# Kernel optimization log

Hardware: AMD Instinct MI355X
Metric: run time of the kernel (lower is better)

## Reference

```python
import jax, jax.numpy as jnp
import numpy as np

PASS = 8        # pass_through_size
FLOW = 16       # flow_size
TRANS = FLOW - PASS  # transform_size = 8
NBINS = 64
HID = 1024


def _conditioner(yA, w1, b1, w2, b2, w3, b3):
    # MLP producing unnormalized positive bin widths Q: [B, TRANS, NBINS]
    h = jax.nn.relu(yA @ w1 + b1)
    h = jax.nn.relu(h @ w2 + b2)
    q = jax.nn.softplus(h @ w3 + b3) + 1e-6  # positivity for slopes
    return q.reshape(-1, TRANS, NBINS)


def setup_inputs() -> dict:
    key = jax.random.key(0)
    ks = jax.random.split(key, 4)
    B = 65536
    y = jax.random.uniform(ks[0], (B, FLOW + 1), dtype=jnp.float32)
    w1 = jax.random.normal(ks[1], (PASS, HID), dtype=jnp.float32) / np.sqrt(PASS)
    w2 = jax.random.normal(ks[2], (HID, HID), dtype=jnp.float32) / np.sqrt(HID)
    w3 = jax.random.normal(ks[3], (HID, TRANS * NBINS), dtype=jnp.float32) / np.sqrt(HID)
    return {
        "y": y,
        "w1": w1, "b1": jnp.zeros((HID,), jnp.float32),
        "w2": w2, "b2": jnp.zeros((HID,), jnp.float32),
        "w3": w3, "b3": jnp.zeros((TRANS * NBINS,), jnp.float32),
    }


def reference(y, w1, b1, w2, b2, w3, b3):
    yA = y[:, :PASS]                      # [B, PASS]
    yB = y[:, PASS:FLOW]                  # [B, TRANS]
    jac = y[:, FLOW:FLOW + 1]             # [B, 1]

    Q = _conditioner(yA, w1, b1, w2, b2, w3, b3)  # [B, TRANS, NBINS]
    Qsum = jnp.cumsum(Q, axis=-1)
    Qnorms = Qsum[:, :, -1:]
    Q = Q / (Qnorms / NBINS)              # slopes per bin
    Qsum = Qsum / Qnorms                  # normalized CDF knots (last == 1)

    # searchsorted(side='left') per row: count of knots strictly below value
    ybins = jnp.sum(Qsum < yB[..., None], axis=-1)          # [B, TRANS] int32
    ybins = jnp.clip(ybins, 0, NBINS - 1)                   # guard fp edge case

    paddedQsum = jnp.pad(Qsum, ((0, 0), (0, 0), (1, 0)))    # prepend 0 knot
    offsets = jnp.take_along_axis(paddedQsum, ybins[..., None], axis=-1)[..., 0]
    slopes = jnp.take_along_axis(Q, ybins[..., None], axis=-1)[..., 0]

    xB = (yB - offsets) / slopes + ybins.astype(jnp.float32) / NBINS
    jac = jac * jnp.prod(1.0 / slopes, axis=-1, keepdims=True)
    return jnp.concatenate((yA, xB, jac), axis=-1)          # [B, FLOW+1]
```

## Files before the change

### kernel.cpp

```cpp
#include <hip/hip_runtime.h>
#include <hip/hip_fp16.h>

#define HID 1024
#define QCOLS 512
#define KP 2048
#define NT 48

typedef _Float16 f16x8 __attribute__((ext_vector_type(8)));
typedef float f32x4 __attribute__((ext_vector_type(4)));

__global__ void tconv_both(const float* __restrict__ w2, __half* __restrict__ w2t,
                           const float* __restrict__ w3, __half* __restrict__ w3t) {
  __shared__ float tile[32][33];
  const int z = blockIdx.z;
  const int N = z ? QCOLS : HID;
  if (blockIdx.x * 32 >= N) return;
  const float* src = z ? w3 : w2;
  __half* dst = z ? w3t : w2t;
  int n0 = blockIdx.x * 32, k0 = blockIdx.y * 32;
  int tx = threadIdx.x, ty = threadIdx.y;
  for (int i = ty; i < 32; i += 8)
    tile[i][tx] = src[(size_t)(k0 + i) * N + n0 + tx];
  __syncthreads();
  for (int i = ty; i < 32; i += 8) {
    float v = tile[tx][i] * 256.f;
    __half h = __float2half(v);
    size_t o = (size_t)(n0 + i) * KP + k0 + tx;
    dst[o] = h;
    dst[o + 1024] = __float2half(v - __half2float(h));
  }
}

__global__ __launch_bounds__(256)
void h1k(const float* __restrict__ y, const float* __restrict__ w1,
         const float* __restrict__ b1, __half* __restrict__ h1,
         int row0, int nrows) {
  const int t = threadIdx.x & 127;
  const int rl = threadIdx.x >> 7;
  const long r = (long)blockIdx.x * 2 + rl;
  if (r >= nrows) return;
  const float* yr = y + (size_t)(row0 + r) * 17;
  float yv[8];
#pragma unroll
  for (int k = 0; k < 8; ++k) yv[k] = yr[k];
  const int c0 = t * 8;
  f32x4 a0 = *(const f32x4*)(b1 + c0);
  f32x4 a1 = *(const f32x4*)(b1 + c0 + 4);
#pragma unroll
  for (int k = 0; k < 8; ++k) {
    const f32x4 w0 = *(const f32x4*)(w1 + k * HID + c0);
    const f32x4 w1v = *(const f32x4*)(w1 + k * HID + c0 + 4);
#pragma unroll
    for (int j = 0; j < 4; ++j) {
      a0[j] = fmaf(yv[k], w0[j], a0[j]);
      a1[j] = fmaf(yv[k], w1v[j], a1[j]);
    }
  }
  f16x8 hi, lo;
#pragma unroll
  for (int j = 0; j < 8; ++j) {
    float v = fmaxf(j < 4 ? a0[j] : a1[j - 4], 0.f) * 64.f;
    _Float16 h = (_Float16)v;
    hi[j] = h;
    lo[j] = (_Float16)(v - (float)h);
  }
  *(f16x8*)(h1 + (size_t)r * KP + c0) = hi;
  *(f16x8*)(h1 + (size_t)r * KP + c0 + 1024) = lo;
}

template <int ACT, int BM, int BN>
__device__ __forceinline__
void gemm1b_body(const __half* __restrict__ A, const __half* __restrict__ Bt,
                 const float* __restrict__ bias, __half* __restrict__ Co,
                 float* __restrict__ Cf, int ldc) {
  constexpr int MFRAG = BM / 32;
  constexpr int NFRAG = BN / 64;
  constexpr int SLOT = (BM + BN) * 64;
  constexpr int LA = BM / 128;
  constexpr int LB = BN / 128;
  constexpr int LPS = LA + LB;
  __shared__ char lds[3 * SLOT];
  const int tid = threadIdx.x;
  const int lane = tid & 63, wave = tid >> 6;
  const int p = lane & 15, ql = lane >> 4;
  const int wm = wave >> 2, wn = wave & 3;

  const int gx = gridDim.x, nwg = gx * gridDim.y;
  const int bid = blockIdx.y * gx + blockIdx.x;
  const int q8 = nwg >> 3, r8 = nwg & 7;
  const int xcd = bid & 7, lxi = bid >> 3;
  const int swz = (xcd < r8 ? xcd * (q8 + 1) : r8 * (q8 + 1) + (xcd - r8) * q8) + lxi;
  const size_t row_blk = (size_t)(swz / gx) * BM;
  const size_t col_blk = (size_t)(swz % gx) * BN;

  int a_off[MFRAG], b_off[NFRAG];
#pragma unroll
  for (int m = 0; m < MFRAG; ++m) {
    int r = wm * (BM / 2) + m * 16 + p;
    a_off[m] = r * 64 + ((ql ^ ((r >> 1) & 3)) << 4);
  }
#pragma unroll
  for (int n = 0; n < NFRAG; ++n) {
    int r = wn * (BN / 4) + n * 16 + p;
    b_off[n] = r * 64 + ((ql ^ ((r >> 1) & 3)) << 4);
  }

  auto gload = [&](const __half* g, char* l) {
    __builtin_amdgcn_global_load_lds((__attribute__((address_space(1))) void*)g,
        (__attribute__((address_space(3))) void*)l, 16, 0, 0);
  };

  auto stage = [&](int q, int slot) {
    int kt = q >> 1; if (kt > NT - 1) kt = NT - 1;
    const int h = q & 1;
    const int lk = kt * 64;
    const int ak = ((lk >= 2048) ? 1024 : 0) + (lk & 1023) + h * 32;
    const int bk = ((lk >= 1024 && lk < 2048) ? 1024 : 0) + (lk & 1023) + h * 32;
    char* pa = lds + slot * SLOT;
    char* pb = pa + BM * 64;
#pragma unroll
    for (int i = 0; i < LA; ++i) {
      const int idx = tid + i * 512;
      const int sr = idx >> 2, sq = (idx & 3) ^ ((sr >> 1) & 3);
      gload(A + (row_blk + sr) * (size_t)KP + ak + sq * 8, pa + idx * 16);
    }
#pragma unroll
    for (int i = 0; i < LB; ++i) {
      const int idx = tid + i * 512;
      const int sr = idx >> 2, sq = (idx & 3) ^ ((sr >> 1) & 3);
      gload(Bt + (col_blk + sr) * (size_t)KP + bk + sq * 8, pb + idx * 16);
    }
  };

  stage(0, 0);
  stage(1, 1);
  if constexpr (LPS == 4) asm volatile("s_waitcnt vmcnt(4)" ::: "memory");
  else                    asm volatile("s_waitcnt vmcnt(3)" ::: "memory");
  __builtin_amdgcn_sched_barrier(0);
  __builtin_amdgcn_s_barrier();
  __builtin_amdgcn_sched_barrier(0);

  f32x4 acc[MFRAG][NFRAG] = {};

  int cur = 0;
  for (int ph = 0; ph < NT * 2; ++ph) {
    const char* base = lds + cur * SLOT;
    const char* pB = base + BM * 64;
    f16x8 af[MFRAG], bfr[NFRAG];
#pragma unroll
    for (int m = 0; m < MFRAG; ++m) af[m] = *(const f16x8*)(base + a_off[m]);
#pragma unroll
    for (int n = 0; n < NFRAG; ++n) bfr[n] = *(const f16x8*)(pB + b_off[n]);
    const int nslot = cur == 0 ? 2 : cur - 1;
    stage(ph + 2, nslot);
    __builtin_amdgcn_sched_barrier(0);
    __builtin_amdgcn_s_barrier();
    __builtin_amdgcn_sched_barrier(0);

    __builtin_amdgcn_s_setprio(1);
#pragma unroll
    for (int m = 0; m < MFRAG; ++m)
#pragma unroll
      for (int n = 0; n < NFRAG; ++n)
        acc[m][n] = __builtin_amdgcn_mfma_f32_16x16x32_f16(af[m], bfr[n], acc[m][n], 0, 0, 0);
    __builtin_amdgcn_s_setprio(0);

    if constexpr (LPS == 4) asm volatile("s_waitcnt vmcnt(4)" ::: "memory");
    else                    asm volatile("s_waitcnt vmcnt(3)" ::: "memory");
    __builtin_amdgcn_sched_barrier(0);
    __builtin_amdgcn_s_barrier();
    __builtin_amdgcn_sched_barrier(0);
    cur = cur == 2 ? 0 : cur + 1;
  }

  const float unscale = 1.f / 16384.f;
#pragma unroll
  for (int n = 0; n < NFRAG; ++n) {
    const size_t col = col_blk + wn * (BN / 4) + n * 16 + p;
    const float bv = bias[col];
#pragma unroll
    for (int m = 0; m < MFRAG; ++m) {
      const size_t row0 = row_blk + wm * (BM / 2) + m * 16 + ql * 4;
#pragma unroll
      for (int j = 0; j < 4; ++j) {
        float v = acc[m][n][j] * unscale + bv;
        const size_t o = (row0 + j) * (size_t)ldc + col;
        if constexpr (ACT == 0) {
          float r = fmaxf(v, 0.f) * 64.f;
          __half hh = __float2half(r);
          Co[o] = hh;
          Co[o + 1024] = __float2half(r - __half2float(hh));
        } else {
          float sp = fmaxf(v, 0.f) + log1pf(expf(-fabsf(v)));
          Cf[o] = sp + 1e-6f;
        }
      }
    }
  }
}

__global__ __launch_bounds__(512, 2)
void g2relu(const __half* __restrict__ A, const __half* __restrict__ B,
            const float* __restrict__ bias, __half* __restrict__ Co) {
  gemm1b_body<0, 256, 256>(A, B, bias, Co, nullptr, KP);
}

__global__ __launch_bounds__(512, 4)
void g3soft(const __half* __restrict__ A, const __half* __restrict__ B,
            const float* __restrict__ bias, float* __restrict__ Cf) {
  gemm1b_body<1, 128, 256>(A, B, bias, nullptr, Cf, QCOLS);
}

__global__ __launch_bounds__(256)
void pwl_epi(const float* __restrict__ y, const float* __restrict__ q,
             float* __restrict__ out, int row0, int nrows) {
  const int wave = threadIdx.x >> 6, lane = threadIdx.x & 63;
  const int r = blockIdx.x * 4 + wave;
  if (r >= nrows) return;
  const float* yr = y + (size_t)(row0 + r) * 17;
  float* orow = out + (size_t)(row0 + r) * 17;
  const float* qr = q + (size_t)r * QCOLS;
  float prod_inv = 1.f;
#pragma unroll
  for (int t = 0; t < 8; ++t) {
    const float qv = qr[t * 64 + lane];
    float s = qv;
#pragma unroll
    for (int d = 1; d < 64; d <<= 1) {
      float u = __shfl_up(s, d);
      if (lane >= d) s += u;
    }
    const float total = __shfl(s, 63);
    const float sn = s / total;
    const float dnorm = total * 0.015625f;
    const float slope_l = qv / dnorm;
    const float yb = yr[8 + t];
    const unsigned long long m = __ballot(sn < yb);
    int bin = (int)__popcll(m);
    bin = bin > 63 ? 63 : bin;
    const float off_g = __shfl(sn, bin > 0 ? bin - 1 : 0);
    const float off = (bin == 0) ? 0.f : off_g;
    const float sl = __shfl(slope_l, bin);
    const float xB = (yb - off) / sl + (float)bin * 0.015625f;
    if (lane == t) orow[8 + t] = xB;
    prod_inv *= (1.f / sl);
  }
  if (lane < 8) orow[lane] = yr[lane];
  if (lane == 8) orow[16] = yr[16] * prod_inv;
}

extern "C" void kernel_launch(void* const* d_in, const int* in_sizes, int n_in,
                              void* d_out, int out_size, void* d_ws, size_t ws_size,
                              hipStream_t stream) {
  const float* y  = (const float*)d_in[0];
  const float* w1 = (const float*)d_in[1];
  const float* b1 = (const float*)d_in[2];
  const float* w2 = (const float*)d_in[3];
  const float* b2 = (const float*)d_in[4];
  const float* w3 = (const float*)d_in[5];
  const float* b3 = (const float*)d_in[6];
  float* out = (float*)d_out;
  const long Btot = in_sizes[0] / 17;

  char* ws = (char*)d_ws;
  __half* w2t = (__half*)ws;
  __half* w3t = (__half*)(ws + (4u << 20));
  const size_t fixed = (size_t)6 << 20;

  const size_t avail = ws_size > fixed ? ws_size - fixed : 0;
  long maxrows = (long)(avail / 8192);
  long chunk = 256;
  for (long c = 65536; c >= 256; c >>= 1) {
    if (c <= maxrows && c <= Btot) { chunk = c; break; }
  }

  __half* h1buf = (__half*)(ws + fixed);
  __half* h2buf = (__half*)(ws + fixed + (size_t)chunk * 4096);
  float* qbuf = (float*)h1buf;

  tconv_both<<<dim3(32, 32, 2), dim3(32, 8), 0, stream>>>(w2, w2t, w3, w3t);

  for (long row0 = 0; row0 < Btot; row0 += chunk) {
    const int nr = (int)((Btot - row0 < chunk) ? (Btot - row0) : chunk);
    h1k<<<(nr + 1) / 2, 256, 0, stream>>>(y, w1, b1, h1buf, (int)row0, nr);
    g2relu<<<dim3(HID / 256, nr / 256), 512, 0, stream>>>(h1buf, w2t, b2, h2buf);
    g3soft<<<dim3(QCOLS / 256, nr / 128), 512, 0, stream>>>(h2buf, w3t, b3, qbuf);
    pwl_epi<<<(nr + 3) / 4, 256, 0, stream>>>(y, qbuf, out, (int)row0, nr);
  }
}
```

Measured before the change: 920.5 us.

## Load B operand directly from global into registers, double-buffered, bypassing LDS

The GEMM body now stages only the A tile through LDS via the triple-buffered global_load_lds ring. Each wave loads its B fragments straight from global memory into registers, one phase ahead, using ping-pong register buffers. This shrinks LDS use and removes the LDS reads for B. In exchange, B data is no longer shared across the waves in a workgroup (the two wm rows fetch duplicate loads), which raises register pressure and global traffic. g3soft's launch bounds drop from 4 to 2 waves per SIMD.

```diff
diff --git a/kernel.cpp b/kernel.cpp
--- a/kernel.cpp
+++ b/kernel.cpp
@@ -70,15 +70,13 @@
 
 template <int ACT, int BM, int BN>
 __device__ __forceinline__
-void gemm1b_body(const __half* __restrict__ A, const __half* __restrict__ Bt,
-                 const float* __restrict__ bias, __half* __restrict__ Co,
-                 float* __restrict__ Cf, int ldc) {
+void gemm_bl2_body(const __half* __restrict__ A, const __half* __restrict__ Bt,
+                   const float* __restrict__ bias, __half* __restrict__ Co,
+                   float* __restrict__ Cf, int ldc) {
   constexpr int MFRAG = BM / 32;
   constexpr int NFRAG = BN / 64;
-  constexpr int SLOT = (BM + BN) * 64;
+  constexpr int SLOT = BM * 64;
   constexpr int LA = BM / 128;
-  constexpr int LB = BN / 128;
-  constexpr int LPS = LA + LB;
   __shared__ char lds[3 * SLOT];
   const int tid = threadIdx.x;
   const int lane = tid & 63, wave = tid >> 6;
@@ -93,49 +91,50 @@
   const size_t row_blk = (size_t)(swz / gx) * BM;
   const size_t col_blk = (size_t)(swz % gx) * BN;
 
-  int a_off[MFRAG], b_off[NFRAG];
+  int a_off[MFRAG];
 #pragma unroll
   for (int m = 0; m < MFRAG; ++m) {
     int r = wm * (BM / 2) + m * 16 + p;
     a_off[m] = r * 64 + ((ql ^ ((r >> 1) & 3)) << 4);
   }
-#pragma unroll
-  for (int n = 0; n < NFRAG; ++n) {
-    int r = wn * (BN / 4) + n * 16 + p;
-    b_off[n] = r * 64 + ((ql ^ ((r >> 1) & 3)) << 4);
-  }
 
   auto gload = [&](const __half* g, char* l) {
     __builtin_amdgcn_global_load_lds((__attribute__((address_space(1))) void*)g,
         (__attribute__((address_space(3))) void*)l, 16, 0, 0);
   };
 
-  auto stage = [&](int q, int slot) {
+  auto stageA = [&](int q, int slot) {
     int kt = q >> 1; if (kt > NT - 1) kt = NT - 1;
     const int h = q & 1;
     const int lk = kt * 64;
     const int ak = ((lk >= 2048) ? 1024 : 0) + (lk & 1023) + h * 32;
-    const int bk = ((lk >= 1024 && lk < 2048) ? 1024 : 0) + (lk & 1023) + h * 32;
     char* pa = lds + slot * SLOT;
-    char* pb = pa + BM * 64;
 #pragma unroll
     for (int i = 0; i < LA; ++i) {
       const int idx = tid + i * 512;
       const int sr = idx >> 2, sq = (idx & 3) ^ ((sr >> 1) & 3);
       gload(A + (row_blk + sr) * (size_t)KP + ak + sq * 8, pa + idx * 16);
     }
-#pragma unroll
-    for (int i = 0; i < LB; ++i) {
-      const int idx = tid + i * 512;
-      const int sr = idx >> 2, sq = (idx & 3) ^ ((sr >> 1) & 3);
-      gload(Bt + (col_blk + sr) * (size_t)KP + bk + sq * 8, pb + idx * 16);
-    }
-  };
-
-  stage(0, 0);
-  stage(1, 1);
-  if constexpr (LPS == 4) asm volatile("s_waitcnt vmcnt(4)" ::: "memory");
-  else                    asm volatile("s_waitcnt vmcnt(3)" ::: "memory");
+  };
+
+  auto loadB = [&](int q, f16x8 (&dst)[NFRAG]) {
+    int kt = q >> 1; if (kt > NT - 1) kt = NT - 1;
+    const int h = q & 1;
+    const int lk = kt * 64;
+    const int bk = ((lk >= 1024 && lk < 2048) ? 1024 : 0) + (lk & 1023) + h * 32;
+#pragma unroll
+    for (int n = 0; n < NFRAG; ++n) {
+      const size_t row = col_blk + wn * (BN / 4) + n * 16 + p;
+      dst[n] = *(const f16x8*)(Bt + row * (size_t)KP + bk + ql * 8);
+    }
+  };
+
+  f16x8 bp[NFRAG], bq[NFRAG];
+
+  stageA(0, 0);
+  stageA(1, 1);
+  loadB(0, bp);
+  asm volatile("s_waitcnt vmcnt(%0)" :: "n"(LA + NFRAG) : "memory");
   __builtin_amdgcn_sched_barrier(0);
   __builtin_amdgcn_s_barrier();
   __builtin_amdgcn_sched_barrier(0);
@@ -143,34 +142,34 @@
   f32x4 acc[MFRAG][NFRAG] = {};
 
   int cur = 0;
-  for (int ph = 0; ph < NT * 2; ++ph) {
+  auto phase = [&](int ph, const f16x8 (&bC)[NFRAG], f16x8 (&bN)[NFRAG]) {
     const char* base = lds + cur * SLOT;
-    const char* pB = base + BM * 64;
-    f16x8 af[MFRAG], bfr[NFRAG];
+    f16x8 af[MFRAG];
 #pragma unroll
     for (int m = 0; m < MFRAG; ++m) af[m] = *(const f16x8*)(base + a_off[m]);
-#pragma unroll
-    for (int n = 0; n < NFRAG; ++n) bfr[n] = *(const f16x8*)(pB + b_off[n]);
     const int nslot = cur == 0 ? 2 : cur - 1;
-    stage(ph + 2, nslot);
+    stageA(ph + 2, nslot);
+    loadB(ph + 1, bN);
+    asm volatile("s_waitcnt vmcnt(%0)" :: "n"(LA + NFRAG) : "memory");
     __builtin_amdgcn_sched_barrier(0);
     __builtin_amdgcn_s_barrier();
     __builtin_amdgcn_sched_barrier(0);
-
     __builtin_amdgcn_s_setprio(1);
 #pragma unroll
     for (int m = 0; m < MFRAG; ++m)
 #pragma unroll
       for (int n = 0; n < NFRAG; ++n)
-        acc[m][n] = __builtin_amdgcn_mfma_f32_16x16x32_f16(af[m], bfr[n], acc[m][n], 0, 0, 0);
+        acc[m][n] = __builtin_amdgcn_mfma_f32_16x16x32_f16(af[m], bC[n], acc[m][n], 0, 0, 0);
     __builtin_amdgcn_s_setprio(0);
-
-    if constexpr (LPS == 4) asm volatile("s_waitcnt vmcnt(4)" ::: "memory");
-    else                    asm volatile("s_waitcnt vmcnt(3)" ::: "memory");
     __builtin_amdgcn_sched_barrier(0);
     __builtin_amdgcn_s_barrier();
     __builtin_amdgcn_sched_barrier(0);
     cur = cur == 2 ? 0 : cur + 1;
+  };
+
+  for (int ph = 0; ph < NT * 2; ph += 2) {
+    phase(ph, bp, bq);
+    phase(ph + 1, bq, bp);
   }
 
   const float unscale = 1.f / 16384.f;
@@ -202,13 +201,13 @@
 __global__ __launch_bounds__(512, 2)
 void g2relu(const __half* __restrict__ A, const __half* __restrict__ B,
             const float* __restrict__ bias, __half* __restrict__ Co) {
-  gemm1b_body<0, 256, 256>(A, B, bias, Co, nullptr, KP);
-}
-
-__global__ __launch_bounds__(512, 4)
+  gemm_bl2_body<0, 256, 256>(A, B, bias, Co, nullptr, KP);
+}
+
+__global__ __launch_bounds__(512, 2)
 void g3soft(const __half* __restrict__ A, const __half* __restrict__ B,
             const float* __restrict__ bias, float* __restrict__ Cf) {
-  gemm1b_body<1, 128, 256>(A, B, bias, nullptr, Cf, QCOLS);
+  gemm_bl2_body<1, 128, 256>(A, B, bias, nullptr, Cf, QCOLS);
 }
 
 __global__ __launch_bounds__(256)
```

Measured after the change: 1.372 ms. +49.0%, slower.

## Deepen GEMM LDS pipeline to four slots and split MFMA phases for 256-row tiles

Applied to the files above, without the earlier changes.

Restructures the fp16 MFMA GEMM main loop to use four LDS slots with a prefetch depth of three K-halves instead of three slots with depth two. For the 256-row tile, the compute is split into two half-tile MFMA phases, and the B-tile global-to-LDS load is issued between them so loads overlap compute more evenly. Explicit lgkmcnt waits are added, and a fixed vmcnt(6) wait replaces the previous per-config counts. The larger LDS footprint, together with g3soft's launch bound dropping from 4 to 2, lowers possible occupancy for the second GEMM, and the extra barriers add sync overhead.

```diff
diff --git a/kernel.cpp b/kernel.cpp
--- a/kernel.cpp
+++ b/kernel.cpp
@@ -70,16 +70,17 @@
 
 template <int ACT, int BM, int BN>
 __device__ __forceinline__
-void gemm1b_body(const __half* __restrict__ A, const __half* __restrict__ Bt,
-                 const float* __restrict__ bias, __half* __restrict__ Co,
-                 float* __restrict__ Cf, int ldc) {
+void gemm_fp_body(const __half* __restrict__ A, const __half* __restrict__ Bt,
+                  const float* __restrict__ bias, __half* __restrict__ Co,
+                  float* __restrict__ Cf, int ldc) {
   constexpr int MFRAG = BM / 32;
   constexpr int NFRAG = BN / 64;
+  constexpr bool MSPLIT = (MFRAG == 8);
+  constexpr int MH = MSPLIT ? 4 : MFRAG;
   constexpr int SLOT = (BM + BN) * 64;
   constexpr int LA = BM / 128;
   constexpr int LB = BN / 128;
-  constexpr int LPS = LA + LB;
-  __shared__ char lds[3 * SLOT];
+  __shared__ char lds[4 * SLOT];
   const int tid = threadIdx.x;
   const int lane = tid & 63, wave = tid >> 6;
   const int p = lane & 15, ql = lane >> 4;
@@ -110,20 +111,25 @@
         (__attribute__((address_space(3))) void*)l, 16, 0, 0);
   };
 
-  auto stage = [&](int q, int slot) {
-    int kt = q >> 1; if (kt > NT - 1) kt = NT - 1;
-    const int h = q & 1;
-    const int lk = kt * 64;
-    const int ak = ((lk >= 2048) ? 1024 : 0) + (lk & 1023) + h * 32;
-    const int bk = ((lk >= 1024 && lk < 2048) ? 1024 : 0) + (lk & 1023) + h * 32;
+  auto stageA = [&](int Hq) {
+    const int Hc = Hq > 2 * NT - 1 ? 2 * NT - 1 : Hq;
+    const int slot = Hc & 3;
+    const int lk = (Hc >> 1) * 64;
+    const int ak = ((lk >= 2048) ? 1024 : 0) + (lk & 1023) + (Hc & 1) * 32;
     char* pa = lds + slot * SLOT;
-    char* pb = pa + BM * 64;
 #pragma unroll
     for (int i = 0; i < LA; ++i) {
       const int idx = tid + i * 512;
       const int sr = idx >> 2, sq = (idx & 3) ^ ((sr >> 1) & 3);
       gload(A + (row_blk + sr) * (size_t)KP + ak + sq * 8, pa + idx * 16);
     }
+  };
+  auto stageB = [&](int Hq) {
+    const int Hc = Hq > 2 * NT - 1 ? 2 * NT - 1 : Hq;
+    const int slot = Hc & 3;
+    const int lk = (Hc >> 1) * 64;
+    const int bk = ((lk >= 1024 && lk < 2048) ? 1024 : 0) + (lk & 1023) + (Hc & 1) * 32;
+    char* pb = lds + slot * SLOT + BM * 64;
 #pragma unroll
     for (int i = 0; i < LB; ++i) {
       const int idx = tid + i * 512;
@@ -132,45 +138,65 @@
     }
   };
 
-  stage(0, 0);
-  stage(1, 1);
-  if constexpr (LPS == 4) asm volatile("s_waitcnt vmcnt(4)" ::: "memory");
-  else                    asm volatile("s_waitcnt vmcnt(3)" ::: "memory");
+  stageA(0); stageB(0);
+  stageA(1); stageB(1);
+  stageA(2); stageB(2);
+  asm volatile("s_waitcnt vmcnt(%0)" :: "n"(2 * (LA + LB)) : "memory");
   __builtin_amdgcn_sched_barrier(0);
   __builtin_amdgcn_s_barrier();
   __builtin_amdgcn_sched_barrier(0);
 
   f32x4 acc[MFRAG][NFRAG] = {};
 
-  int cur = 0;
-  for (int ph = 0; ph < NT * 2; ++ph) {
-    const char* base = lds + cur * SLOT;
+  for (int H = 0; H < 2 * NT; ++H) {
+    const char* base = lds + (H & 3) * SLOT;
     const char* pB = base + BM * 64;
-    f16x8 af[MFRAG], bfr[NFRAG];
-#pragma unroll
-    for (int m = 0; m < MFRAG; ++m) af[m] = *(const f16x8*)(base + a_off[m]);
+    f16x8 bfr[NFRAG], af[MH];
 #pragma unroll
     for (int n = 0; n < NFRAG; ++n) bfr[n] = *(const f16x8*)(pB + b_off[n]);
-    const int nslot = cur == 0 ? 2 : cur - 1;
-    stage(ph + 2, nslot);
+#pragma unroll
+    for (int m = 0; m < MH; ++m) af[m] = *(const f16x8*)(base + a_off[m]);
+    stageA(H + 3);
+    if constexpr (!MSPLIT) stageB(H + 3);
     __builtin_amdgcn_sched_barrier(0);
     __builtin_amdgcn_s_barrier();
     __builtin_amdgcn_sched_barrier(0);
-
+    asm volatile("s_waitcnt lgkmcnt(0)" ::: "memory");
+    __builtin_amdgcn_sched_barrier(0);
     __builtin_amdgcn_s_setprio(1);
 #pragma unroll
-    for (int m = 0; m < MFRAG; ++m)
+    for (int m = 0; m < MH; ++m)
 #pragma unroll
       for (int n = 0; n < NFRAG; ++n)
         acc[m][n] = __builtin_amdgcn_mfma_f32_16x16x32_f16(af[m], bfr[n], acc[m][n], 0, 0, 0);
     __builtin_amdgcn_s_setprio(0);
 
-    if constexpr (LPS == 4) asm volatile("s_waitcnt vmcnt(4)" ::: "memory");
-    else                    asm volatile("s_waitcnt vmcnt(3)" ::: "memory");
+    if constexpr (MSPLIT) {
+      __builtin_amdgcn_sched_barrier(0);
+      __builtin_amdgcn_s_barrier();
+      __builtin_amdgcn_sched_barrier(0);
+      f16x8 af2[4];
+#pragma unroll
+      for (int m = 0; m < 4; ++m) af2[m] = *(const f16x8*)(base + a_off[4 + m]);
+      stageB(H + 3);
+      __builtin_amdgcn_sched_barrier(0);
+      __builtin_amdgcn_s_barrier();
+      __builtin_amdgcn_sched_barrier(0);
+      asm volatile("s_waitcnt lgkmcnt(0)" ::: "memory");
+      __builtin_amdgcn_sched_barrier(0);
+      __builtin_amdgcn_s_setprio(1);
+#pragma unroll
+      for (int m = 0; m < 4; ++m)
+#pragma unroll
+        for (int n = 0; n < NFRAG; ++n)
+          acc[4 + m][n] = __builtin_amdgcn_mfma_f32_16x16x32_f16(af2[m], bfr[n], acc[4 + m][n], 0, 0, 0);
+      __builtin_amdgcn_s_setprio(0);
+    }
+
+    asm volatile("s_waitcnt vmcnt(6)" ::: "memory");
     __builtin_amdgcn_sched_barrier(0);
     __builtin_amdgcn_s_barrier();
     __builtin_amdgcn_sched_barrier(0);
-    cur = cur == 2 ? 0 : cur + 1;
   }
 
   const float unscale = 1.f / 16384.f;
@@ -202,13 +228,13 @@
 __global__ __launch_bounds__(512, 2)
 void g2relu(const __half* __restrict__ A, const __half* __restrict__ B,
             const float* __restrict__ bias, __half* __restrict__ Co) {
-  gemm1b_body<0, 256, 256>(A, B, bias, Co, nullptr, KP);
-}
-
-__global__ __launch_bounds__(512, 4)
+  gemm_fp_body<0, 256, 256>(A, B, bias, Co, nullptr, KP);
+}
+
+__global__ __launch_bounds__(512, 2)
 void g3soft(const __half* __restrict__ A, const __half* __restrict__ B,
             const float* __restrict__ bias, float* __restrict__ Cf) {
-  gemm1b_body<1, 128, 256>(A, B, bias, nullptr, Cf, QCOLS);
+  gemm_fp_body<1, 128, 256>(A, B, bias, nullptr, Cf, QCOLS);
 }
 
 __global__ __launch_bounds__(256)
```

Result: no change. 911.5 us (-1.0%).
